# Kernel tuning notes

Measured on AMD Instinct MI355X. Metric: run time of the kernel, lower is better.

## Reference

```python
import jax, jax.numpy as jnp
import numpy as np

V, E, H2, K = 30000, 256, 256, 13  # vocab, embed dim, per-direction hidden, num tags
B, T = 64, 512


def setup_inputs() -> dict:
    key = jax.random.key(0)
    ks = jax.random.split(key, 12)
    s = 0.1
    return {
        "x": jax.random.randint(ks[0], (B, T), 0, V, dtype=jnp.int32),
        "emb": jax.random.normal(ks[1], (V, E), dtype=jnp.float32) * s,
        "w_ih_f": jax.random.normal(ks[2], (4 * H2, E), dtype=jnp.float32) * s,
        "w_hh_f": jax.random.normal(ks[3], (4 * H2, H2), dtype=jnp.float32) * s,
        "b_ih_f": jnp.zeros((4 * H2,), jnp.float32),
        "b_hh_f": jnp.zeros((4 * H2,), jnp.float32),
        "w_ih_b": jax.random.normal(ks[4], (4 * H2, E), dtype=jnp.float32) * s,
        "w_hh_b": jax.random.normal(ks[5], (4 * H2, H2), dtype=jnp.float32) * s,
        "b_ih_b": jnp.zeros((4 * H2,), jnp.float32),
        "b_hh_b": jnp.zeros((4 * H2,), jnp.float32),
        "w_out": jax.random.normal(ks[6], (K, 2 * H2), dtype=jnp.float32) * s,
        "b_out": jnp.zeros((K,), jnp.float32),
        "start_trans": jax.random.normal(ks[7], (K,), dtype=jnp.float32) * s,
        "end_trans": jax.random.normal(ks[8], (K,), dtype=jnp.float32) * s,
        "trans": jax.random.normal(ks[9], (K, K), dtype=jnp.float32) * s,
    }


def _lstm_dir(xg, w_hh, reverse):
    # xg: [T, B, 4H] precomputed input-side gate pre-activations (PyTorch i|f|g|o order)
    Bsz, H = xg.shape[1], w_hh.shape[1]

    def step(carry, g_in):
        h, c = carry
        g = g_in + h @ w_hh.T
        i, f, gg, o = jnp.split(g, 4, axis=-1)
        c = jax.nn.sigmoid(f) * c + jax.nn.sigmoid(i) * jnp.tanh(gg)
        h = jax.nn.sigmoid(o) * jnp.tanh(c)
        return (h, c), h

    init = (jnp.zeros((Bsz, H), xg.dtype), jnp.zeros((Bsz, H), xg.dtype))
    _, hs = jax.lax.scan(step, init, xg, reverse=reverse)
    return hs  # [T, B, H]


def reference(x, emb, w_ih_f, w_hh_f, b_ih_f, b_hh_f, w_ih_b, w_hh_b, b_ih_b, b_hh_b,
              w_out, b_out, start_trans, end_trans, trans):
    e = emb[x].transpose(1, 0, 2)                     # [T, B, E] time-major
    xg_f = e @ w_ih_f.T + (b_ih_f + b_hh_f)           # [T, B, 4H] (fold both biases)
    xg_b = e @ w_ih_b.T + (b_ih_b + b_hh_b)
    h_f = _lstm_dir(xg_f, w_hh_f, reverse=False)
    h_b = _lstm_dir(xg_b, w_hh_b, reverse=True)
    h = jnp.concatenate([h_f, h_b], axis=-1)          # [T, B, 2H]; dropout = identity (eval)
    emissions = h @ w_out.T + b_out                   # [T, B, K]

    # CRF Viterbi decode (torchcrf semantics, full mask)
    score = start_trans + emissions[0]                # [B, K]

    def vstep(score, emit_t):
        s = score[:, :, None] + trans[None] + emit_t[:, None, :]  # [B, K_prev, K_next]
        return s.max(axis=1), s.argmax(axis=1)

    score, bps = jax.lax.scan(vstep, score, emissions[1:])        # bps: [T-1, B, K]
    score = score + end_trans
    best_last = jnp.argmax(score, axis=-1)            # [B]
    best_score = jnp.max(score, axis=-1)              # [B]

    def btstep(tag, bp_t):
        prev = jnp.take_along_axis(bp_t, tag[:, None], axis=1)[:, 0]
        return prev, prev

    _, path_head = jax.lax.scan(btstep, best_last, bps, reverse=True)  # [T-1, B]
    path = jnp.concatenate([path_head, best_last[None]], axis=0).T     # [B, T]
    return path, best_score
```

## Files before the change

kernel.cpp:

```cpp
#include <hip/hip_runtime.h>
#include <stdint.h>
#include <stddef.h>

#define T_LEN  512
#define BATCH  64
#define NTAG   13
#define CT     64
#define NCHUNK 8

__device__ __forceinline__ float sigm(float x) { return 1.0f / (1.0f + expf(-x)); }

union __align__(16) SharedU {
    struct {
        float w[32][260];
        float h[16][260];
        float red[7][32][20];
        float gate[32][17];
    } l;
    struct {
        float Wl[16][132];
        float El[16][132];
        int   tok[128];
    } g;
};

__global__ __launch_bounds__(256) void xg_gemm(
    const int* __restrict__ x, const float* __restrict__ emb,
    const float* __restrict__ w_ih_f, const float* __restrict__ w_ih_b,
    const float* __restrict__ b_ih_f, const float* __restrict__ b_hh_f,
    const float* __restrict__ b_ih_b, const float* __restrict__ b_hh_b,
    float* __restrict__ xg_ws, int chunk)
{
    const int tid = threadIdx.x;
    const int mt = blockIdx.x;
    const int nt = blockIdx.y;
    const int d  = blockIdx.z;
    const int tbase = (d == 0 ? chunk : (NCHUNK - 1 - chunk)) * CT;
    const float* W  = (d == 0) ? w_ih_f : w_ih_b;
    const float* bi = (d == 0) ? b_ih_f : b_ih_b;
    const float* bh = (d == 0) ? b_hh_f : b_hh_b;

    __shared__ __align__(16) float Wl[16][132];
    __shared__ __align__(16) float El[16][132];
    __shared__ int tok[128];

    if (tid < 128) {
        int col = nt * 128 + tid;
        tok[tid] = x[(col & 63) * T_LEN + tbase + (col >> 6)];
    }
    __syncthreads();

    const int r  = tid >> 1;
    const int c8 = (tid & 1) * 8;
    const int tm = tid >> 4;
    const int tn = tid & 15;

    float acc[8][8];
#pragma unroll
    for (int i = 0; i < 8; i++)
#pragma unroll
        for (int jz = 0; jz < 8; jz++) acc[i][jz] = 0.0f;

    const float* wrow = &W[(size_t)(mt * 128 + r) * 256];
    const float* erow = &emb[(size_t)tok[r] * 256];

    for (int kb = 0; kb < 256; kb += 16) {
        float4 w0 = *(const float4*)&wrow[kb + c8];
        float4 w1 = *(const float4*)&wrow[kb + c8 + 4];
        float4 e0 = *(const float4*)&erow[kb + c8];
        float4 e1 = *(const float4*)&erow[kb + c8 + 4];
        __syncthreads();
        Wl[c8+0][r] = w0.x; Wl[c8+1][r] = w0.y; Wl[c8+2][r] = w0.z; Wl[c8+3][r] = w0.w;
        Wl[c8+4][r] = w1.x; Wl[c8+5][r] = w1.y; Wl[c8+6][r] = w1.z; Wl[c8+7][r] = w1.w;
        El[c8+0][r] = e0.x; El[c8+1][r] = e0.y; El[c8+2][r] = e0.z; El[c8+3][r] = e0.w;
        El[c8+4][r] = e1.x; El[c8+5][r] = e1.y; El[c8+6][r] = e1.z; El[c8+7][r] = e1.w;
        __syncthreads();
#pragma unroll
        for (int kk = 0; kk < 16; kk++) {
            float a[8], b[8];
            *(float4*)&a[0] = *(const float4*)&Wl[kk][tm*8];
            *(float4*)&a[4] = *(const float4*)&Wl[kk][tm*8+4];
            *(float4*)&b[0] = *(const float4*)&El[kk][tn*8];
            *(float4*)&b[4] = *(const float4*)&El[kk][tn*8+4];
#pragma unroll
            for (int i = 0; i < 8; i++)
#pragma unroll
                for (int jz = 0; jz < 8; jz++)
                    acc[i][jz] += a[i] * b[jz];
        }
    }

    const int colbase = nt * 128 + tn * 8;
    const int j  = colbase >> 6;
    const int b0 = colbase & 63;
#pragma unroll
    for (int gi = 0; gi < 8; gi++) {
        int g = mt * 128 + tm * 8 + gi;
        float bias = bi[g] + bh[g];
        float* dst = &xg_ws[(((size_t)(d * CT + j) * 1024 + g) << 6) + b0];
        float4 v0 = make_float4(acc[gi][0]+bias, acc[gi][1]+bias, acc[gi][2]+bias, acc[gi][3]+bias);
        float4 v1 = make_float4(acc[gi][4]+bias, acc[gi][5]+bias, acc[gi][6]+bias, acc[gi][7]+bias);
        *(float4*)dst       = v0;
        *(float4*)(dst + 4) = v1;
    }
}

__global__ __launch_bounds__(256) void fused_chunk(
    const float* __restrict__ xg_ws_c, float* __restrict__ xg_ws_w,
    const float* __restrict__ w_hh_f, const float* __restrict__ w_hh_b,
    float* h_ex, float* c_state, float* h_all, int* flags,
    const int* __restrict__ x, const float* __restrict__ emb,
    const float* __restrict__ w_ih_f, const float* __restrict__ w_ih_b,
    const float* __restrict__ b_ih_f, const float* __restrict__ b_hh_f,
    const float* __restrict__ b_ih_b, const float* __restrict__ b_hh_b,
    int chunk)
{
    __shared__ SharedU smem;
    const int tid = threadIdx.x;
    const int bid = blockIdx.x;

    if (bid < 256) {
        __builtin_amdgcn_s_setprio(3);
        const int dg    = bid & 7;
        const int slice = bid >> 3;
        const int dir = dg & 1;
        const int grp = dg >> 1;
        const int h_base = slice * 8;
        const int sbase  = grp * 16;

        const float* W = dir ? w_hh_b : w_hh_f;
        for (int idx = tid; idx < 2048; idx += 256) {
            int f  = idx << 2;
            int rr = f >> 8;
            int c4 = f & 255;
            int row = (rr >> 3) * 256 + h_base + (rr & 7);
            *(float4*)&smem.l.w[rr][c4] = *(const float4*)&W[(size_t)row * 256 + c4];
        }

        const int ih_g = tid & 7;
        const int s_g  = tid >> 3;
        float c_val = 0.0f;
        if (tid < 128)
            c_val = c_state[(size_t)(dir * 64 + sbase + s_g) * 256 + h_base + ih_g];

        {
            const float* base = &h_ex[((size_t)dg * 16) * 256];
#pragma unroll
            for (int i = 0; i < 8; i++) {
                int pos = tid + 256 * i;
                int fo  = pos << 1;
                unsigned long long u64 = __hip_atomic_load(
                    (const unsigned long long*)(base + fo), __ATOMIC_RELAXED, __HIP_MEMORY_SCOPE_AGENT);
                float2 v = __builtin_bit_cast(float2, u64);
                *(float2*)&smem.l.h[fo >> 8][fo & 255] = v;
            }
        }
        __syncthreads();

        const int kc   = tid >> 5;
        const int tile = tid & 31;
        const int gt = tile >> 2;
        const int st = tile & 3;
        const float* wr[4] = { &smem.l.w[gt][0], &smem.l.w[8+gt][0], &smem.l.w[16+gt][0], &smem.l.w[24+gt][0] };
        const float* hr[4] = { &smem.l.h[st][0], &smem.l.h[4+st][0], &smem.l.h[8+st][0],  &smem.l.h[12+st][0] };

        float hv_prev = 0.0f;
        size_t ha_prev = 0;

#pragma unroll 1
        for (int tl = 0; tl < CT; tl++) {
            const int jslot = dir ? (CT - 1 - tl) : tl;
            const int t = (dir ? (NCHUNK - 1 - chunk) : chunk) * CT + jslot;
            const int sc = chunk * CT + tl + 1;
            const int par = sc & 1;

            float xg0 = 0.f, xg1 = 0.f, xg2 = 0.f, xg3 = 0.f;
            if (tid < 128) {
                if (tl > 0) h_all[ha_prev] = hv_prev;
                const float* xp = &xg_ws_c[(((size_t)(dir * CT + jslot) * 1024) + h_base + ih_g) * 64 + sbase + s_g];
                xg0 = xp[0];
                xg1 = xp[1 * 256 * 64];
                xg2 = xp[2 * 256 * 64];
                xg3 = xp[3 * 256 * 64];
            }

            float acc[4][4];
#pragma unroll
            for (int gi = 0; gi < 4; gi++)
#pragma unroll
                for (int si = 0; si < 4; si++) acc[gi][si] = 0.0f;

            const int j0 = kc * 32;
#pragma unroll
            for (int m = 0; m < 8; m++) {
                const int jj = j0 + m * 4;
                float4 w4[4], h4[4];
#pragma unroll
                for (int i = 0; i < 4; i++) w4[i] = *(const float4*)(wr[i] + jj);
#pragma unroll
                for (int i = 0; i < 4; i++) h4[i] = *(const float4*)(hr[i] + jj);
#pragma unroll
                for (int gi = 0; gi < 4; gi++)
#pragma unroll
                    for (int si = 0; si < 4; si++)
                        acc[gi][si] += w4[gi].x*h4[si].x + w4[gi].y*h4[si].y
                                     + w4[gi].z*h4[si].z + w4[gi].w*h4[si].w;
            }

            if (kc >= 1) {
#pragma unroll
                for (int gi = 0; gi < 4; gi++)
                    *(float4*)&smem.l.red[kc-1][tile][gi*4] =
                        make_float4(acc[gi][0], acc[gi][1], acc[gi][2], acc[gi][3]);
            }
            __syncthreads();
            if (kc == 0) {
#pragma unroll
                for (int p = 0; p < 7; p++)
#pragma unroll
                    for (int gi = 0; gi < 4; gi++) {
                        float4 v = *(const float4*)&smem.l.red[p][tile][gi*4];
                        acc[gi][0] += v.x; acc[gi][1] += v.y; acc[gi][2] += v.z; acc[gi][3] += v.w;
                    }
#pragma unroll
                for (int gi = 0; gi < 4; gi++)
#pragma unroll
                    for (int si = 0; si < 4; si++)
                        smem.l.gate[8*gi + gt][4*si + st] = acc[gi][si];
            }
            __syncthreads();

            if (tid < 128) {
                float gI = smem.l.gate[     ih_g][s_g] + xg0;
                float gF = smem.l.gate[8  + ih_g][s_g] + xg1;
                float gG = smem.l.gate[16 + ih_g][s_g] + xg2;
                float gO = smem.l.gate[24 + ih_g][s_g] + xg3;
                c_val = sigm(gF) * c_val + sigm(gI) * tanhf(gG);
                float hv = sigm(gO) * tanhf(c_val);
                __hip_atomic_store(&h_ex[(((size_t)par * 8 + dg) * 16 + s_g) * 256 + h_base + ih_g],
                                   hv, __ATOMIC_RELAXED, __HIP_MEMORY_SCOPE_AGENT);
                hv_prev = hv;
                ha_prev = ((size_t)t * 64 + sbase + s_g) * 512 + dir * 256 + h_base + ih_g;
            }
            __syncthreads();

            if (tid == 0)
                __hip_atomic_store(&flags[dg * 32 + slice], sc, __ATOMIC_RELAXED, __HIP_MEMORY_SCOPE_AGENT);

            if (tid < 64) {
                const int* fp = &flags[dg * 32 + (tid & 31)];
                int spins = 0;
                int v = __hip_atomic_load(fp, __ATOMIC_RELAXED, __HIP_MEMORY_SCOPE_AGENT);
                while (__ballot(v < sc) != 0ull) {
                    if (++spins > 8) __builtin_amdgcn_s_sleep(1);
                    v = __hip_atomic_load(fp, __ATOMIC_RELAXED, __HIP_MEMORY_SCOPE_AGENT);
                    if (spins > (1 << 20)) break;
                }
            }
            __syncthreads();

            {
                const float* base = &h_ex[(((size_t)par * 8 + dg) * 16) * 256];
#pragma unroll
                for (int i = 0; i < 8; i++) {
                    int pos = tid + 256 * i;
                    int fo  = pos << 1;
                    unsigned long long u64 = __hip_atomic_load(
                        (const unsigned long long*)(base + fo), __ATOMIC_RELAXED, __HIP_MEMORY_SCOPE_AGENT);
                    float2 v = __builtin_bit_cast(float2, u64);
                    *(float2*)&smem.l.h[fo >> 8][fo & 255] = v;
                }
            }
            __syncthreads();
        }

        if (tid < 128) {
            h_all[ha_prev] = hv_prev;
            c_state[(size_t)(dir * 64 + sbase + s_g) * 256 + h_base + ih_g] = c_val;
        }
    } else {
        if (chunk == NCHUNK - 1) return;
        const int v  = bid - 256;
        const int mt = v & 7;
        const int nt = (v >> 3) & 31;
        const int d  = v >> 8;
        const int cn = chunk + 1;
        const int tbase = (d == 0 ? cn : (NCHUNK - 1 - cn)) * CT;
        const float* W  = (d == 0) ? w_ih_f : w_ih_b;
        const float* bi = (d == 0) ? b_ih_f : b_ih_b;
        const float* bh = (d == 0) ? b_hh_f : b_hh_b;

        if (tid < 128) {
            int col = nt * 128 + tid;
            smem.g.tok[tid] = x[(col & 63) * T_LEN + tbase + (col >> 6)];
        }
        __syncthreads();

        const int r  = tid >> 1;
        const int c8 = (tid & 1) * 8;
        const int tm = tid >> 4;
        const int tn = tid & 15;

        float acc[8][8];
#pragma unroll
        for (int i = 0; i < 8; i++)
#pragma unroll
            for (int jz = 0; jz < 8; jz++) acc[i][jz] = 0.0f;

        const float* wrow = &W[(size_t)(mt * 128 + r) * 256];
        const float* erow = &emb[(size_t)smem.g.tok[r] * 256];

        for (int kb = 0; kb < 256; kb += 16) {
            float4 w0 = *(const float4*)&wrow[kb + c8];
            float4 w1 = *(const float4*)&wrow[kb + c8 + 4];
            float4 e0 = *(const float4*)&erow[kb + c8];
            float4 e1 = *(const float4*)&erow[kb + c8 + 4];
            __syncthreads();
            smem.g.Wl[c8+0][r] = w0.x; smem.g.Wl[c8+1][r] = w0.y; smem.g.Wl[c8+2][r] = w0.z; smem.g.Wl[c8+3][r] = w0.w;
            smem.g.Wl[c8+4][r] = w1.x; smem.g.Wl[c8+5][r] = w1.y; smem.g.Wl[c8+6][r] = w1.z; smem.g.Wl[c8+7][r] = w1.w;
            smem.g.El[c8+0][r] = e0.x; smem.g.El[c8+1][r] = e0.y; smem.g.El[c8+2][r] = e0.z; smem.g.El[c8+3][r] = e0.w;
            smem.g.El[c8+4][r] = e1.x; smem.g.El[c8+5][r] = e1.y; smem.g.El[c8+6][r] = e1.z; smem.g.El[c8+7][r] = e1.w;
            __syncthreads();
#pragma unroll
            for (int kk = 0; kk < 16; kk++) {
                float a[8], b[8];
                *(float4*)&a[0] = *(const float4*)&smem.g.Wl[kk][tm*8];
                *(float4*)&a[4] = *(const float4*)&smem.g.Wl[kk][tm*8+4];
                *(float4*)&b[0] = *(const float4*)&smem.g.El[kk][tn*8];
                *(float4*)&b[4] = *(const float4*)&smem.g.El[kk][tn*8+4];
#pragma unroll
                for (int i = 0; i < 8; i++)
#pragma unroll
                    for (int jz = 0; jz < 8; jz++)
                        acc[i][jz] += a[i] * b[jz];
            }
        }

        {
            const int target = (d == 0) ? (chunk * CT + 2 * nt + 2)
                                        : (chunk * CT + CT - 2 * nt);
            if (tid < 64) {
                const int l = tid;
                const int* f0 = &flags[(d + 2 * (l >> 5)) * 32 + (l & 31)];
                const int* f1 = &flags[(d + 2 * ((l >> 5) + 2)) * 32 + (l & 31)];
                int spins = 0;
                for (;;) {
                    int a0 = __hip_atomic_load(f0, __ATOMIC_RELAXED, __HIP_MEMORY_SCOPE_AGENT);
                    int a1 = __hip_atomic_load(f1, __ATOMIC_RELAXED, __HIP_MEMORY_SCOPE_AGENT);
                    if (__ballot(a0 < target || a1 < target) == 0ull) break;
                    __builtin_amdgcn_s_sleep(8);
                    if (++spins > (1 << 20)) break;
                }
            }
            __syncthreads();
        }

        const int colbase = nt * 128 + tn * 8;
        const int j  = colbase >> 6;
        const int b0 = colbase & 63;
#pragma unroll
        for (int gi = 0; gi < 8; gi++) {
            int g = mt * 128 + tm * 8 + gi;
            float bias = bi[g] + bh[g];
            float* dst = &xg_ws_w[(((size_t)(d * CT + j) * 1024 + g) << 6) + b0];
            float4 v0 = make_float4(acc[gi][0]+bias, acc[gi][1]+bias, acc[gi][2]+bias, acc[gi][3]+bias);
            float4 v1 = make_float4(acc[gi][4]+bias, acc[gi][5]+bias, acc[gi][6]+bias, acc[gi][7]+bias);
            *(float4*)dst       = v0;
            *(float4*)(dst + 4) = v1;
        }
    }
}

__global__ __launch_bounds__(256) void emis_kernel(
    const float* __restrict__ h_all, const float* __restrict__ w_out,
    const float* __restrict__ b_out, float* __restrict__ emis)
{
    const int row = blockIdx.x * 16 + (threadIdx.x >> 4);
    const int k   = threadIdx.x & 15;
    const float* hr = &h_all[(size_t)row * 512];
    const float* wr = &w_out[(size_t)(k < NTAG ? k : 0) * 512];
    float acc = 0.0f;
#pragma unroll 8
    for (int e = 0; e < 512; e += 4) {
        float4 h4 = *(const float4*)&hr[e];
        float4 w4 = *(const float4*)&wr[e];
        acc += h4.x*w4.x + h4.y*w4.y + h4.z*w4.z + h4.w*w4.w;
    }
    if (k < NTAG) emis[(size_t)row * NTAG + k] = acc + b_out[k];
}

__global__ __launch_bounds__(64) void viterbi_kernel(
    const float* __restrict__ emis, const float* __restrict__ start_trans,
    const float* __restrict__ end_trans, const float* __restrict__ trans,
    float* __restrict__ out)
{
    const int b = blockIdx.x;
    const int k = threadIdx.x;
    __shared__ float em[T_LEN * NTAG];
    __shared__ unsigned char bp[T_LEN][16];

    for (int t = k; t < T_LEN; t += 64) {
        const float* src = &emis[((size_t)t * 64 + b) * NTAG];
#pragma unroll
        for (int kk = 0; kk < NTAG; kk++)
            em[t * NTAG + kk] = src[kk];
    }
    __syncthreads();

    float tc[NTAG];
#pragma unroll
    for (int kp = 0; kp < NTAG; kp++)
        tc[kp] = (k < NTAG) ? trans[kp * NTAG + k] : 0.0f;

    float score = (k < NTAG) ? (start_trans[k] + em[k]) : -3.0e38f;

    for (int t = 1; t < T_LEN; t++) {
        float best = -3.0e38f;
        int bi = 0;
#pragma unroll
        for (int kp = 0; kp < NTAG; kp++) {
            float v = __shfl(score, kp) + tc[kp];
            if (v > best) { best = v; bi = kp; }
        }
        if (k < NTAG) {
            score = best + em[t * NTAG + k];
            bp[t][k] = (unsigned char)bi;
        }
    }
    if (k < NTAG) score += end_trans[k];
    else score = -3.0e38f;
    __syncthreads();

    float bs = -3.0e38f;
    int tag = 0;
#pragma unroll
    for (int kk = 0; kk < NTAG; kk++) {
        float v = __shfl(score, kk);
        if (v > bs) { bs = v; tag = kk; }
    }
    if (k == 0) {
        out[32768 + b] = bs;
        int tg = tag;
        out[b * T_LEN + (T_LEN - 1)] = (float)tg;
        for (int t = T_LEN - 1; t >= 1; t--) {
            tg = bp[t][tg];
            out[b * T_LEN + t - 1] = (float)tg;
        }
    }
}

extern "C" void kernel_launch(void* const* d_in, const int* in_sizes, int n_in,
                              void* d_out, int out_size, void* d_ws, size_t ws_size,
                              hipStream_t stream)
{
    (void)in_sizes; (void)n_in; (void)out_size; (void)ws_size;
    const int*   x    = (const int*)  d_in[0];
    const float* emb  = (const float*)d_in[1];
    const float* wihf = (const float*)d_in[2];
    const float* whhf = (const float*)d_in[3];
    const float* bihf = (const float*)d_in[4];
    const float* bhhf = (const float*)d_in[5];
    const float* wihb = (const float*)d_in[6];
    const float* whhb = (const float*)d_in[7];
    const float* bihb = (const float*)d_in[8];
    const float* bhhb = (const float*)d_in[9];
    const float* wout = (const float*)d_in[10];
    const float* bout = (const float*)d_in[11];
    const float* stt  = (const float*)d_in[12];
    const float* ent  = (const float*)d_in[13];
    const float* trn  = (const float*)d_in[14];
    float* out = (float*)d_out;

    char* ws = (char*)d_ws;
    size_t off = 0;
    float* xg_ws = (float*)(ws + off); off += (size_t)2 * CT * 1024 * 64 * 4;
    float* h_all = (float*)(ws + off); off += (size_t)T_LEN * 64 * 512 * 4;
    float* h_ex  = (float*)(ws + off); off += (size_t)2 * 8 * 16 * 256 * 4;
    float* c_st  = (float*)(ws + off); off += (size_t)2 * 64 * 256 * 4;
    float* emis  = (float*)(ws + off); off += (size_t)T_LEN * 64 * NTAG * 4;
    int*   flags = (int*)  (ws + off); off += 8 * 32 * 4;

    hipMemsetAsync(h_ex,  0, (size_t)2 * 8 * 16 * 256 * 4, stream);
    hipMemsetAsync(c_st,  0, (size_t)2 * 64 * 256 * 4, stream);
    hipMemsetAsync(flags, 0, 8 * 32 * 4, stream);

    xg_gemm<<<dim3(8, 32, 2), 256, 0, stream>>>(x, emb, wihf, wihb,
                                                bihf, bhhf, bihb, bhhb, xg_ws, 0);
    for (int c = 0; c < NCHUNK; c++) {
        fused_chunk<<<768, 256, 0, stream>>>(xg_ws, xg_ws, whhf, whhb,
                                             h_ex, c_st, h_all, flags,
                                             x, emb, wihf, wihb,
                                             bihf, bhhf, bihb, bhhb, c);
    }
    emis_kernel<<<2048, 256, 0, stream>>>(h_all, wout, bout, emis);
    viterbi_kernel<<<64, 64, 0, stream>>>(emis, stt, ent, trn, out);
}
```

Baseline: 3.586 ms.

## Process both LSTM directions per recurrent block and shrink the grid

Result: slower. 6.172 ms (+72.1%).

```diff
diff --git a/kernel.cpp b/kernel.cpp
--- a/kernel.cpp
+++ b/kernel.cpp
@@ -12,8 +12,8 @@
 
 union __align__(16) SharedU {
     struct {
-        float w[32][260];
-        float h[16][260];
+        float w[2][32][260];
+        float h[2][16][260];
         float red[7][32][20];
         float gate[32][17];
     } l;
@@ -119,32 +119,35 @@
     const int tid = threadIdx.x;
     const int bid = blockIdx.x;
 
-    if (bid < 256) {
-        __builtin_amdgcn_s_setprio(3);
-        const int dg    = bid & 7;
-        const int slice = bid >> 3;
-        const int dir = dg & 1;
-        const int grp = dg >> 1;
+    if (bid < 128) {
+        const int g     = bid & 3;
+        const int slice = bid >> 2;
         const int h_base = slice * 8;
-        const int sbase  = grp * 16;
-
-        const float* W = dir ? w_hh_b : w_hh_f;
-        for (int idx = tid; idx < 2048; idx += 256) {
-            int f  = idx << 2;
-            int rr = f >> 8;
-            int c4 = f & 255;
-            int row = (rr >> 3) * 256 + h_base + (rr & 7);
-            *(float4*)&smem.l.w[rr][c4] = *(const float4*)&W[(size_t)row * 256 + c4];
+        const int sbase  = g * 16;
+
+#pragma unroll
+        for (int dir = 0; dir < 2; dir++) {
+            const float* W = dir ? w_hh_b : w_hh_f;
+            for (int idx = tid; idx < 2048; idx += 256) {
+                int f  = idx << 2;
+                int rr = f >> 8;
+                int c4 = f & 255;
+                int row = (rr >> 3) * 256 + h_base + (rr & 7);
+                *(float4*)&smem.l.w[dir][rr][c4] = *(const float4*)&W[(size_t)row * 256 + c4];
+            }
         }
 
         const int ih_g = tid & 7;
         const int s_g  = tid >> 3;
-        float c_val = 0.0f;
-        if (tid < 128)
-            c_val = c_state[(size_t)(dir * 64 + sbase + s_g) * 256 + h_base + ih_g];
-
-        {
-            const float* base = &h_ex[((size_t)dg * 16) * 256];
+        float c_val[2] = {0.0f, 0.0f};
+        if (tid < 128) {
+            c_val[0] = c_state[(size_t)(      sbase + s_g) * 256 + h_base + ih_g];
+            c_val[1] = c_state[(size_t)(64 +  sbase + s_g) * 256 + h_base + ih_g];
+        }
+
+#pragma unroll
+        for (int dir = 0; dir < 2; dir++) {
+            const float* base = &h_ex[((size_t)(dir * 4 + g) * 16) * 256];
 #pragma unroll
             for (int i = 0; i < 8; i++) {
                 int pos = tid + 256 * i;
@@ -152,7 +155,7 @@
                 unsigned long long u64 = __hip_atomic_load(
                     (const unsigned long long*)(base + fo), __ATOMIC_RELAXED, __HIP_MEMORY_SCOPE_AGENT);
                 float2 v = __builtin_bit_cast(float2, u64);
-                *(float2*)&smem.l.h[fo >> 8][fo & 255] = v;
+                *(float2*)&smem.l.h[dir][fo >> 8][fo & 255] = v;
             }
         }
         __syncthreads();
@@ -161,106 +164,114 @@
         const int tile = tid & 31;
         const int gt = tile >> 2;
         const int st = tile & 3;
-        const float* wr[4] = { &smem.l.w[gt][0], &smem.l.w[8+gt][0], &smem.l.w[16+gt][0], &smem.l.w[24+gt][0] };
-        const float* hr[4] = { &smem.l.h[st][0], &smem.l.h[4+st][0], &smem.l.h[8+st][0],  &smem.l.h[12+st][0] };
-
-        float hv_prev = 0.0f;
-        size_t ha_prev = 0;
+
+        float hv_prev[2] = {0.0f, 0.0f};
+        size_t ha_prev[2] = {0, 0};
 
 #pragma unroll 1
         for (int tl = 0; tl < CT; tl++) {
-            const int jslot = dir ? (CT - 1 - tl) : tl;
-            const int t = (dir ? (NCHUNK - 1 - chunk) : chunk) * CT + jslot;
-            const int sc = chunk * CT + tl + 1;
+            const int sc  = chunk * CT + tl + 1;
             const int par = sc & 1;
 
-            float xg0 = 0.f, xg1 = 0.f, xg2 = 0.f, xg3 = 0.f;
-            if (tid < 128) {
-                if (tl > 0) h_all[ha_prev] = hv_prev;
-                const float* xp = &xg_ws_c[(((size_t)(dir * CT + jslot) * 1024) + h_base + ih_g) * 64 + sbase + s_g];
-                xg0 = xp[0];
-                xg1 = xp[1 * 256 * 64];
-                xg2 = xp[2 * 256 * 64];
-                xg3 = xp[3 * 256 * 64];
-            }
-
-            float acc[4][4];
-#pragma unroll
-            for (int gi = 0; gi < 4; gi++)
-#pragma unroll
-                for (int si = 0; si < 4; si++) acc[gi][si] = 0.0f;
-
-            const int j0 = kc * 32;
-#pragma unroll
-            for (int m = 0; m < 8; m++) {
-                const int jj = j0 + m * 4;
-                float4 w4[4], h4[4];
-#pragma unroll
-                for (int i = 0; i < 4; i++) w4[i] = *(const float4*)(wr[i] + jj);
-#pragma unroll
-                for (int i = 0; i < 4; i++) h4[i] = *(const float4*)(hr[i] + jj);
+#pragma unroll
+            for (int dir = 0; dir < 2; dir++) {
+                const int jslot = dir ? (CT - 1 - tl) : tl;
+                const int t = (dir ? (NCHUNK - 1 - chunk) : chunk) * CT + jslot;
+
+                float xg0 = 0.f, xg1 = 0.f, xg2 = 0.f, xg3 = 0.f;
+                if (tid < 128) {
+                    if (tl > 0) h_all[ha_prev[dir]] = hv_prev[dir];
+                    const float* xp = &xg_ws_c[(((size_t)(dir * CT + jslot) * 1024) + h_base + ih_g) * 64 + sbase + s_g];
+                    xg0 = xp[0];
+                    xg1 = xp[1 * 256 * 64];
+                    xg2 = xp[2 * 256 * 64];
+                    xg3 = xp[3 * 256 * 64];
+                }
+
+                float acc[4][4];
 #pragma unroll
                 for (int gi = 0; gi < 4; gi++)
 #pragma unroll
-                    for (int si = 0; si < 4; si++)
-                        acc[gi][si] += w4[gi].x*h4[si].x + w4[gi].y*h4[si].y
-                                     + w4[gi].z*h4[si].z + w4[gi].w*h4[si].w;
-            }
-
-            if (kc >= 1) {
-#pragma unroll
-                for (int gi = 0; gi < 4; gi++)
-                    *(float4*)&smem.l.red[kc-1][tile][gi*4] =
-                        make_float4(acc[gi][0], acc[gi][1], acc[gi][2], acc[gi][3]);
-            }
-            __syncthreads();
-            if (kc == 0) {
-#pragma unroll
-                for (int p = 0; p < 7; p++)
-#pragma unroll
-                    for (int gi = 0; gi < 4; gi++) {
-                        float4 v = *(const float4*)&smem.l.red[p][tile][gi*4];
-                        acc[gi][0] += v.x; acc[gi][1] += v.y; acc[gi][2] += v.z; acc[gi][3] += v.w;
+                    for (int si = 0; si < 4; si++) acc[gi][si] = 0.0f;
+
+                const float* wr[4] = { &smem.l.w[dir][gt][0],    &smem.l.w[dir][8+gt][0],
+                                       &smem.l.w[dir][16+gt][0], &smem.l.w[dir][24+gt][0] };
+                const float* hr[4] = { &smem.l.h[dir][st][0],    &smem.l.h[dir][4+st][0],
+                                       &smem.l.h[dir][8+st][0],  &smem.l.h[dir][12+st][0] };
+
+                const int j0 = kc * 32;
+#pragma unroll
+                for (int m = 0; m < 8; m++) {
+                    const int jj = j0 + m * 4;
+                    float4 w4[4], h4[4];
+#pragma unroll
+                    for (int i = 0; i < 4; i++) w4[i] = *(const float4*)(wr[i] + jj);
+#pragma unroll
+                    for (int i = 0; i < 4; i++) h4[i] = *(const float4*)(hr[i] + jj);
+#pragma unroll
+                    for (int gi = 0; gi < 4; gi++)
+#pragma unroll
+                        for (int si = 0; si < 4; si++)
+                            acc[gi][si] += w4[gi].x*h4[si].x + w4[gi].y*h4[si].y
+                                         + w4[gi].z*h4[si].z + w4[gi].w*h4[si].w;
+                }
+
+                if (kc >= 1) {
+#pragma unroll
+                    for (int gi = 0; gi < 4; gi++)
+                        *(float4*)&smem.l.red[kc-1][tile][gi*4] =
+                            make_float4(acc[gi][0], acc[gi][1], acc[gi][2], acc[gi][3]);
+                }
+                __syncthreads();
+                if (kc == 0) {
+#pragma unroll
+                    for (int p = 0; p < 7; p++)
+#pragma unroll
+                        for (int gi = 0; gi < 4; gi++) {
+                            float4 v = *(const float4*)&smem.l.red[p][tile][gi*4];
+                            acc[gi][0] += v.x; acc[gi][1] += v.y; acc[gi][2] += v.z; acc[gi][3] += v.w;
+                        }
+#pragma unroll
+                    for (int gi = 0; gi < 4; gi++)
+#pragma unroll
+                        for (int si = 0; si < 4; si++)
+                            smem.l.gate[8*gi + gt][4*si + st] = acc[gi][si];
+                }
+                __syncthreads();
+
+                if (tid < 128) {
+                    float gI = smem.l.gate[     ih_g][s_g] + xg0;
+                    float gF = smem.l.gate[8  + ih_g][s_g] + xg1;
+                    float gG = smem.l.gate[16 + ih_g][s_g] + xg2;
+                    float gO = smem.l.gate[24 + ih_g][s_g] + xg3;
+                    c_val[dir] = sigm(gF) * c_val[dir] + sigm(gI) * tanhf(gG);
+                    float hv = sigm(gO) * tanhf(c_val[dir]);
+                    __hip_atomic_store(
+                        &h_ex[(((size_t)par * 8 + dir * 4 + g) * 16 + s_g) * 256 + h_base + ih_g],
+                        hv, __ATOMIC_RELAXED, __HIP_MEMORY_SCOPE_AGENT);
+                    hv_prev[dir] = hv;
+                    ha_prev[dir] = ((size_t)t * 64 + sbase + s_g) * 512 + dir * 256 + h_base + ih_g;
+                }
+                __syncthreads();
+                if (tid == 0)
+                    __hip_atomic_store(&flags[dir * 128 + g * 32 + slice], sc,
+                                       __ATOMIC_RELAXED, __HIP_MEMORY_SCOPE_AGENT);
+            }
+
+#pragma unroll
+            for (int dir = 0; dir < 2; dir++) {
+                if (tid < 64) {
+                    const int* fp = &flags[dir * 128 + g * 32 + (tid & 31)];
+                    int spins = 0;
+                    int v = __hip_atomic_load(fp, __ATOMIC_RELAXED, __HIP_MEMORY_SCOPE_AGENT);
+                    while (__ballot(v < sc) != 0ull) {
+                        if (++spins > 8) __builtin_amdgcn_s_sleep(1);
+                        v = __hip_atomic_load(fp, __ATOMIC_RELAXED, __HIP_MEMORY_SCOPE_AGENT);
+                        if (spins > (1 << 20)) break;
                     }
-#pragma unroll
-                for (int gi = 0; gi < 4; gi++)
-#pragma unroll
-                    for (int si = 0; si < 4; si++)
-                        smem.l.gate[8*gi + gt][4*si + st] = acc[gi][si];
-            }
-            __syncthreads();
-
-            if (tid < 128) {
-                float gI = smem.l.gate[     ih_g][s_g] + xg0;
-                float gF = smem.l.gate[8  + ih_g][s_g] + xg1;
-                float gG = smem.l.gate[16 + ih_g][s_g] + xg2;
-                float gO = smem.l.gate[24 + ih_g][s_g] + xg3;
-                c_val = sigm(gF) * c_val + sigm(gI) * tanhf(gG);
-                float hv = sigm(gO) * tanhf(c_val);
-                __hip_atomic_store(&h_ex[(((size_t)par * 8 + dg) * 16 + s_g) * 256 + h_base + ih_g],
-                                   hv, __ATOMIC_RELAXED, __HIP_MEMORY_SCOPE_AGENT);
-                hv_prev = hv;
-                ha_prev = ((size_t)t * 64 + sbase + s_g) * 512 + dir * 256 + h_base + ih_g;
-            }
-            __syncthreads();
-
-            if (tid == 0)
-                __hip_atomic_store(&flags[dg * 32 + slice], sc, __ATOMIC_RELAXED, __HIP_MEMORY_SCOPE_AGENT);
-
-            if (tid < 64) {
-                const int* fp = &flags[dg * 32 + (tid & 31)];
-                int spins = 0;
-                int v = __hip_atomic_load(fp, __ATOMIC_RELAXED, __HIP_MEMORY_SCOPE_AGENT);
-                while (__ballot(v < sc) != 0ull) {
-                    if (++spins > 8) __builtin_amdgcn_s_sleep(1);
-                    v = __hip_atomic_load(fp, __ATOMIC_RELAXED, __HIP_MEMORY_SCOPE_AGENT);
-                    if (spins > (1 << 20)) break;
-                }
-            }
-            __syncthreads();
-
-            {
-                const float* base = &h_ex[(((size_t)par * 8 + dg) * 16) * 256];
+                }
+                __syncthreads();
+                const float* base = &h_ex[(((size_t)par * 8 + dir * 4 + g) * 16) * 256];
 #pragma unroll
                 for (int i = 0; i < 8; i++) {
                     int pos = tid + 256 * i;
@@ -268,22 +279,24 @@
                     unsigned long long u64 = __hip_atomic_load(
                         (const unsigned long long*)(base + fo), __ATOMIC_RELAXED, __HIP_MEMORY_SCOPE_AGENT);
                     float2 v = __builtin_bit_cast(float2, u64);
-                    *(float2*)&smem.l.h[fo >> 8][fo & 255] = v;
+                    *(float2*)&smem.l.h[dir][fo >> 8][fo & 255] = v;
                 }
             }
             __syncthreads();
         }
 
         if (tid < 128) {
-            h_all[ha_prev] = hv_prev;
-            c_state[(size_t)(dir * 64 + sbase + s_g) * 256 + h_base + ih_g] = c_val;
+            h_all[ha_prev[0]] = hv_prev[0];
+            h_all[ha_prev[1]] = hv_prev[1];
+            c_state[(size_t)(     sbase + s_g) * 256 + h_base + ih_g] = c_val[0];
+            c_state[(size_t)(64 + sbase + s_g) * 256 + h_base + ih_g] = c_val[1];
         }
     } else {
         if (chunk == NCHUNK - 1) return;
-        const int v  = bid - 256;
-        const int mt = v & 7;
-        const int nt = (v >> 3) & 31;
-        const int d  = v >> 8;
+        const int v    = bid - 128;
+        const int d    = v & 1;
+        const int nt   = (v >> 1) & 31;
+        const int half = v >> 6;
         const int cn = chunk + 1;
         const int tbase = (d == 0 ? cn : (NCHUNK - 1 - cn)) * CT;
         const float* W  = (d == 0) ? w_ih_f : w_ih_b;
@@ -300,73 +313,75 @@
         const int c8 = (tid & 1) * 8;
         const int tm = tid >> 4;
         const int tn = tid & 15;
-
-        float acc[8][8];
-#pragma unroll
-        for (int i = 0; i < 8; i++)
-#pragma unroll
-            for (int jz = 0; jz < 8; jz++) acc[i][jz] = 0.0f;
-
-        const float* wrow = &W[(size_t)(mt * 128 + r) * 256];
         const float* erow = &emb[(size_t)smem.g.tok[r] * 256];
 
-        for (int kb = 0; kb < 256; kb += 16) {
-            float4 w0 = *(const float4*)&wrow[kb + c8];
-            float4 w1 = *(const float4*)&wrow[kb + c8 + 4];
-            float4 e0 = *(const float4*)&erow[kb + c8];
-            float4 e1 = *(const float4*)&erow[kb + c8 + 4];
-            __syncthreads();
-            smem.g.Wl[c8+0][r] = w0.x; smem.g.Wl[c8+1][r] = w0.y; smem.g.Wl[c8+2][r] = w0.z; smem.g.Wl[c8+3][r] = w0.w;
-            smem.g.Wl[c8+4][r] = w1.x; smem.g.Wl[c8+5][r] = w1.y; smem.g.Wl[c8+6][r] = w1.z; smem.g.Wl[c8+7][r] = w1.w;
-            smem.g.El[c8+0][r] = e0.x; smem.g.El[c8+1][r] = e0.y; smem.g.El[c8+2][r] = e0.z; smem.g.El[c8+3][r] = e0.w;
-            smem.g.El[c8+4][r] = e1.x; smem.g.El[c8+5][r] = e1.y; smem.g.El[c8+6][r] = e1.z; smem.g.El[c8+7][r] = e1.w;
-            __syncthreads();
-#pragma unroll
-            for (int kk = 0; kk < 16; kk++) {
-                float a[8], b[8];
-                *(float4*)&a[0] = *(const float4*)&smem.g.Wl[kk][tm*8];
-                *(float4*)&a[4] = *(const float4*)&smem.g.Wl[kk][tm*8+4];
-                *(float4*)&b[0] = *(const float4*)&smem.g.El[kk][tn*8];
-                *(float4*)&b[4] = *(const float4*)&smem.g.El[kk][tn*8+4];
-#pragma unroll
-                for (int i = 0; i < 8; i++)
-#pragma unroll
-                    for (int jz = 0; jz < 8; jz++)
-                        acc[i][jz] += a[i] * b[jz];
-            }
-        }
-
-        {
-            const int target = (d == 0) ? (chunk * CT + 2 * nt + 2)
-                                        : (chunk * CT + CT - 2 * nt);
-            if (tid < 64) {
-                const int l = tid;
-                const int* f0 = &flags[(d + 2 * (l >> 5)) * 32 + (l & 31)];
-                const int* f1 = &flags[(d + 2 * ((l >> 5) + 2)) * 32 + (l & 31)];
-                int spins = 0;
-                for (;;) {
-                    int a0 = __hip_atomic_load(f0, __ATOMIC_RELAXED, __HIP_MEMORY_SCOPE_AGENT);
-                    int a1 = __hip_atomic_load(f1, __ATOMIC_RELAXED, __HIP_MEMORY_SCOPE_AGENT);
-                    if (__ballot(a0 < target || a1 < target) == 0ull) break;
-                    __builtin_amdgcn_s_sleep(8);
-                    if (++spins > (1 << 20)) break;
-                }
-            }
-            __syncthreads();
-        }
-
-        const int colbase = nt * 128 + tn * 8;
-        const int j  = colbase >> 6;
-        const int b0 = colbase & 63;
-#pragma unroll
-        for (int gi = 0; gi < 8; gi++) {
-            int g = mt * 128 + tm * 8 + gi;
-            float bias = bi[g] + bh[g];
-            float* dst = &xg_ws_w[(((size_t)(d * CT + j) * 1024 + g) << 6) + b0];
-            float4 v0 = make_float4(acc[gi][0]+bias, acc[gi][1]+bias, acc[gi][2]+bias, acc[gi][3]+bias);
-            float4 v1 = make_float4(acc[gi][4]+bias, acc[gi][5]+bias, acc[gi][6]+bias, acc[gi][7]+bias);
-            *(float4*)dst       = v0;
-            *(float4*)(dst + 4) = v1;
+#pragma unroll 1
+        for (int mt = half * 4; mt < half * 4 + 4; mt++) {
+            float acc[8][8];
+#pragma unroll
+            for (int i = 0; i < 8; i++)
+#pragma unroll
+                for (int jz = 0; jz < 8; jz++) acc[i][jz] = 0.0f;
+
+            const float* wrow = &W[(size_t)(mt * 128 + r) * 256];
+
+            for (int kb = 0; kb < 256; kb += 16) {
+                float4 w0 = *(const float4*)&wrow[kb + c8];
+                float4 w1 = *(const float4*)&wrow[kb + c8 + 4];
+                float4 e0 = *(const float4*)&erow[kb + c8];
+                float4 e1 = *(const float4*)&erow[kb + c8 + 4];
+                __syncthreads();
+                smem.g.Wl[c8+0][r] = w0.x; smem.g.Wl[c8+1][r] = w0.y; smem.g.Wl[c8+2][r] = w0.z; smem.g.Wl[c8+3][r] = w0.w;
+                smem.g.Wl[c8+4][r] = w1.x; smem.g.Wl[c8+5][r] = w1.y; smem.g.Wl[c8+6][r] = w1.z; smem.g.Wl[c8+7][r] = w1.w;
+                smem.g.El[c8+0][r] = e0.x; smem.g.El[c8+1][r] = e0.y; smem.g.El[c8+2][r] = e0.z; smem.g.El[c8+3][r] = e0.w;
+                smem.g.El[c8+4][r] = e1.x; smem.g.El[c8+5][r] = e1.y; smem.g.El[c8+6][r] = e1.z; smem.g.El[c8+7][r] = e1.w;
+                __syncthreads();
+#pragma unroll
+                for (int kk = 0; kk < 16; kk++) {
+                    float a[8], b[8];
+                    *(float4*)&a[0] = *(const float4*)&smem.g.Wl[kk][tm*8];
+                    *(float4*)&a[4] = *(const float4*)&smem.g.Wl[kk][tm*8+4];
+                    *(float4*)&b[0] = *(const float4*)&smem.g.El[kk][tn*8];
+                    *(float4*)&b[4] = *(const float4*)&smem.g.El[kk][tn*8+4];
+#pragma unroll
+                    for (int i = 0; i < 8; i++)
+#pragma unroll
+                        for (int jz = 0; jz < 8; jz++)
+                            acc[i][jz] += a[i] * b[jz];
+                }
+            }
+
+            if (mt == half * 4) {
+                const int target = (d == 0) ? (chunk * CT + 2 * nt + 2)
+                                            : (chunk * CT + CT - 2 * nt);
+                if (tid < 64) {
+                    const int* f0 = &flags[d * 128 + tid];
+                    const int* f1 = &flags[d * 128 + 64 + tid];
+                    int spins = 0;
+                    for (;;) {
+                        int a0 = __hip_atomic_load(f0, __ATOMIC_RELAXED, __HIP_MEMORY_SCOPE_AGENT);
+                        int a1 = __hip_atomic_load(f1, __ATOMIC_RELAXED, __HIP_MEMORY_SCOPE_AGENT);
+                        if (__ballot(a0 < target || a1 < target) == 0ull) break;
+                        __builtin_amdgcn_s_sleep(8);
+                        if (++spins > (1 << 20)) break;
+                    }
+                }
+                __syncthreads();
+            }
+
+            const int colbase = nt * 128 + tn * 8;
+            const int j  = colbase >> 6;
+            const int b0 = colbase & 63;
+#pragma unroll
+            for (int gi = 0; gi < 8; gi++) {
+                int gg = mt * 128 + tm * 8 + gi;
+                float bias = bi[gg] + bh[gg];
+                float* dst = &xg_ws_w[(((size_t)(d * CT + j) * 1024 + gg) << 6) + b0];
+                float4 v0 = make_float4(acc[gi][0]+bias, acc[gi][1]+bias, acc[gi][2]+bias, acc[gi][3]+bias);
+                float4 v1 = make_float4(acc[gi][4]+bias, acc[gi][5]+bias, acc[gi][6]+bias, acc[gi][7]+bias);
+                *(float4*)dst       = v0;
+                *(float4*)(dst + 4) = v1;
+            }
         }
     }
 }
@@ -478,16 +493,16 @@
     float* h_ex  = (float*)(ws + off); off += (size_t)2 * 8 * 16 * 256 * 4;
     float* c_st  = (float*)(ws + off); off += (size_t)2 * 64 * 256 * 4;
     float* emis  = (float*)(ws + off); off += (size_t)T_LEN * 64 * NTAG * 4;
-    int*   flags = (int*)  (ws + off); off += 8 * 32 * 4;
+    int*   flags = (int*)  (ws + off); off += 256 * 4;
 
     hipMemsetAsync(h_ex,  0, (size_t)2 * 8 * 16 * 256 * 4, stream);
     hipMemsetAsync(c_st,  0, (size_t)2 * 64 * 256 * 4, stream);
-    hipMemsetAsync(flags, 0, 8 * 32 * 4, stream);
+    hipMemsetAsync(flags, 0, 256 * 4, stream);
 
     xg_gemm<<<dim3(8, 32, 2), 256, 0, stream>>>(x, emb, wihf, wihb,
                                                 bihf, bhhf, bihb, bhhb, xg_ws, 0);
     for (int c = 0; c < NCHUNK; c++) {
-        fused_chunk<<<768, 256, 0, stream>>>(xg_ws, xg_ws, whhf, whhb,
+        fused_chunk<<<256, 256, 0, stream>>>(xg_ws, xg_ws, whhf, whhb,
                                              h_ex, c_st, h_all, flags,
                                              x, emb, wihf, wihb,
                                              bihf, bhhf, bihb, bhhb, c);
```
